# Kernel optimization log

Hardware: AMD Instinct MI355X
Metric: run time of the kernel (lower is better)

The kernel has to match this reference:

```python
import jax, jax.numpy as jnp
import numpy as np
import math

MUL = 32
E = 131072
N = 10000
IRREPS = [(0, 1), (1, -1), (2, 1)]  # (l, parity) for 0e + 1o + 2e
SQRT3 = math.sqrt(3.0)

_f = math.factorial


def _w3j_symbol(j1, j2, j3, m1, m2, m3):
    """Standard (complex-basis) Wigner 3j symbol via the Racah formula."""
    if m1 + m2 + m3 != 0:
        return 0.0
    if abs(m1) > j1 or abs(m2) > j2 or abs(m3) > j3:
        return 0.0
    if not (abs(j1 - j2) <= j3 <= j1 + j2):
        return 0.0
    tri = _f(j1 + j2 - j3) * _f(j1 - j2 + j3) * _f(-j1 + j2 + j3) / _f(j1 + j2 + j3 + 1)
    pref = (-1) ** (j1 - j2 - m3) * math.sqrt(
        tri * _f(j1 + m1) * _f(j1 - m1) * _f(j2 + m2) * _f(j2 - m2) * _f(j3 + m3) * _f(j3 - m3)
    )
    tmin = max(0, j2 - j3 - m1, j1 - j3 + m2)
    tmax = min(j1 + j2 - j3, j1 - m1, j2 + m2)
    s = 0.0
    for t in range(tmin, tmax + 1):
        s += (-1) ** t / (
            _f(t) * _f(j3 - j2 + t + m1) * _f(j3 - j1 + t - m2)
            * _f(j1 + j2 - j3 - t) * _f(j1 - t - m1) * _f(j2 - t + m2)
        )
    return pref * s


def _real_basis(l):
    """Complex -> real spherical-harmonic change of basis, rows m=-l..l."""
    U = np.zeros((2 * l + 1, 2 * l + 1), dtype=np.complex128)
    U[l, l] = 1.0
    s = 1.0 / math.sqrt(2.0)
    for m in range(1, l + 1):
        U[l + m, l + m] = ((-1) ** m) * s
        U[l + m, l - m] = s
        U[l - m, l - m] = 1j * s
        U[l - m, l + m] = -1j * ((-1) ** m) * s
    return U


def _w3j_real(l1, l2, l3):
    """Real-basis Wigner 3j tensor, Frobenius norm 1 (e3nn normalization)."""
    Wc = np.zeros((2 * l1 + 1, 2 * l2 + 1, 2 * l3 + 1), dtype=np.complex128)
    for m1 in range(-l1, l1 + 1):
        for m2 in range(-l2, l2 + 1):
            for m3 in range(-l3, l3 + 1):
                Wc[l1 + m1, l2 + m2, l3 + m3] = _w3j_symbol(l1, l2, l3, m1, m2, m3)
    C = np.einsum('im,jn,ko,mno->ijk', _real_basis(l1), _real_basis(l2), _real_basis(l3), Wc)
    re, im = C.real, C.imag
    R = re if np.linalg.norm(re) >= np.linalg.norm(im) else im
    return R / np.linalg.norm(R)


def _build_w3j():
    dims = [2 * l + 1 for l, _ in IRREPS]
    offs = np.concatenate([[0], np.cumsum(dims)])[:-1]
    base_dim = int(sum(dims))  # 9
    # auto-generated instructions: same loop order as the torch module
    ins = []
    for io, (lo, po) in enumerate(IRREPS):
        for i1, (l1, p1) in enumerate(IRREPS):
            for i2, (l2, p2) in enumerate(IRREPS):
                if p1 * p2 == po and abs(l1 - l2) <= lo <= l1 + l2:
                    ins.append((i1, i2, io))
    P = len(ins)  # 11 paths
    w3j = np.zeros((P, base_dim, base_dim, base_dim), dtype=np.float32)
    for p, (i1, i2, io) in enumerate(ins):
        l1, l2, lo = IRREPS[i1][0], IRREPS[i2][0], IRREPS[io][0]
        C = _w3j_real(l1, l2, lo) * math.sqrt(2 * lo + 1)  # component normalization
        w3j[p, offs[i1]:offs[i1] + dims[i1], offs[i2]:offs[i2] + dims[i2], offs[io]:offs[io] + dims[io]] = C
    return w3j


def setup_inputs() -> dict:
    key = jax.random.key(0)
    k1, k2, k3, k4 = jax.random.split(key, 4)
    w3j = jnp.asarray(_build_w3j())  # [P=11, 9, 9, 9]
    P = w3j.shape[0]
    base_dim = w3j.shape[1]
    return {
        'x1': jax.random.normal(k1, (E, MUL * base_dim), dtype=jnp.float32),
        'x2': jax.random.normal(k2, (E, MUL * base_dim), dtype=jnp.float32),
        'idxs': jax.random.randint(k3, (E,), 0, N),
        'weights': jax.random.uniform(k4, (MUL, P), dtype=jnp.float32, minval=-SQRT3, maxval=SQRT3),
        'w3j': w3j,
        'scatter_dim_size': N,
    }


def reference(x1, x2, idxs, weights, w3j, scatter_dim_size):
    base1 = w3j.shape[1]
    base2 = w3j.shape[2]
    # scatter edges -> nodes, then gather back per edge (neighbor sum per center)
    x2s = jax.ops.segment_sum(x2, idxs, num_segments=int(scatter_dim_size))
    x2g = x2s[idxs]
    x1r = x1.reshape(-1, MUL, base1)   # [E, u, i]
    x2r = x2g.reshape(-1, MUL, base2)  # [E, u, j]
    # path-channel coupled weighting: 'up,pijk->uijk'
    ww3j = jnp.einsum('up,pijk->uijk', weights, w3j)
    # out[e,u,k] = sum_ij x1[e,u,i] x2[e,u,j] ww3j[u,i,j,k]
    out = jnp.einsum('eui,euj,uijk->euk', x1r, x2r, ww3j)
    return out
```

## Files before the change

kernel.cpp:

```cpp
#include <hip/hip_runtime.h>

#define MULV 32
#define BASE 9
#define ROW 288
#define NPATH 11
#define W3J_SZ 729
#define PACK_STRIDE 96
#define PACK_TOTAL (MULV * PACK_STRIDE)
#define TILE 64
#define QCOL 72
#define LSTR 73
#define NQ4 18
#define QTOT (TILE * NQ4)

typedef float f4a4 __attribute__((ext_vector_type(4), aligned(4)));

__device__ constexpr int p_o1[NPATH] = {0,1,4, 0,1,1,4, 0,1,4,4};
__device__ constexpr int p_d1[NPATH] = {1,3,5, 1,3,3,5, 1,3,5,5};
__device__ constexpr int p_o2[NPATH] = {0,1,4, 1,0,4,1, 4,1,0,4};
__device__ constexpr int p_d2[NPATH] = {1,3,5, 3,1,5,3, 5,3,1,5};
__device__ constexpr int p_o3[NPATH] = {0,0,0, 1,1,1,1, 4,4,4,4};
__device__ constexpr int p_d3[NPATH] = {1,1,1, 3,3,3,3, 5,5,5,5};
__device__ constexpr int p_l1[NPATH] = {0,1,2, 0,1,1,2, 0,1,2,2};
__device__ constexpr int p_l2[NPATH] = {0,1,2, 1,0,2,1, 2,1,0,2};
__device__ constexpr int p_l3[NPATH] = {0,0,0, 1,1,1,1, 2,2,2,2};

__device__ __host__ constexpr bool cell_nz(int p, int i, int j, int k) {
    int m1 = i - p_l1[p], m2 = j - p_l2[p], m3 = k - p_l3[p];
    if ((((m1 < 0) + (m2 < 0) + (m3 < 0)) & 1) != 0) return false;
    int a1 = m1 < 0 ? -m1 : m1, a2 = m2 < 0 ? -m2 : m2, a3 = m3 < 0 ? -m3 : m3;
    int d = a1 - a2; if (d < 0) d = -d;
    return (a3 == a1 + a2) || (a3 == d);
}
__device__ __host__ constexpr bool pair_nz(int p, int i, int j) {
    for (int k = 0; k < p_d3[p]; ++k) if (cell_nz(p, i, j, k)) return true;
    return false;
}


__global__ void zero_count_kernel(float* __restrict__ ws, const int* __restrict__ dN) {
    int N = dN[0];
    int* count = (int*)(ws + PACK_TOTAL + (long)N * ROW);
    for (int i = blockIdx.x * blockDim.x + threadIdx.x; i < N; i += gridDim.x * blockDim.x)
        count[i] = 0;
}

__global__ void hist_kernel(const int* __restrict__ idxs, float* __restrict__ ws,
                            const int* __restrict__ dN, int E) {
    int N = dN[0];
    int* count = (int*)(ws + PACK_TOTAL + (long)N * ROW);
    int t = blockIdx.x * blockDim.x + threadIdx.x;
    if (t < E) atomicAdd(&count[idxs[t]], 1);
}

__global__ void scan_kernel(float* __restrict__ ws, const int* __restrict__ dN) {
    int N = dN[0];
    int* count  = (int*)(ws + PACK_TOTAL + (long)N * ROW);
    int* offset = count + N;
    int* cursor = count + 2 * N;
    __shared__ int tsum[1024];
    const int tid = threadIdx.x;
    int cpt = (N + 1023) / 1024;
    int lo = tid * cpt;
    int hi = lo + cpt; if (hi > N) hi = N;
    int s = 0;
    for (int i = lo; i < hi; ++i) s += count[i];
    int v = s;
    tsum[tid] = v;
    __syncthreads();
    #pragma unroll
    for (int off = 1; off < 1024; off <<= 1) {
        int t = (tid >= off) ? tsum[tid - off] : 0;
        __syncthreads();
        v += t;
        tsum[tid] = v;
        __syncthreads();
    }
    int run = v - s;
    for (int i = lo; i < hi; ++i) {
        int c = count[i];
        offset[i] = run; cursor[i] = run;
        run += c;
    }
}

__global__ void fill_kernel(const int* __restrict__ idxs, float* __restrict__ ws,
                            const int* __restrict__ dN, int E) {
    int N = dN[0];
    int* count  = (int*)(ws + PACK_TOTAL + (long)N * ROW);
    int* cursor = count + 2 * N;
    int* bucket = count + 3 * N;
    int t = blockIdx.x * blockDim.x + threadIdx.x;
    if (t < E) {
        int n = idxs[t];
        int pos = atomicAdd(&cursor[n], 1);
        bucket[pos] = t;
    }
}

__global__ __launch_bounds__(256) void gather_sum_kernel(const float* __restrict__ x2,
                                                         float* __restrict__ ws,
                                                         const int* __restrict__ dN) {
    int N = dN[0];
    float* x2s  = ws + PACK_TOTAL;
    int* count  = (int*)(x2s + (long)N * ROW);
    int* offset = count + N;
    int* bucket = count + 3 * N;
    const int lane = threadIdx.x & 63;
    const int wv   = threadIdx.x >> 6;
    for (int n0 = blockIdx.x * 4 + wv; n0 < N; n0 += gridDim.x * 4) {
        int n   = __builtin_amdgcn_readfirstlane(n0);
        int off = offset[n];
        int deg = count[n];
        float4 a0 = make_float4(0.f, 0.f, 0.f, 0.f);
        float4 a1 = make_float4(0.f, 0.f, 0.f, 0.f);
        int d = 0;
        for (; d + 4 <= deg; d += 4) {
            int e0 = bucket[off + d + 0];
            int e1 = bucket[off + d + 1];
            int e2 = bucket[off + d + 2];
            int e3 = bucket[off + d + 3];
            const float4* r0 = (const float4*)(x2 + (long)e0 * ROW);
            const float4* r1 = (const float4*)(x2 + (long)e1 * ROW);
            const float4* r2 = (const float4*)(x2 + (long)e2 * ROW);
            const float4* r3 = (const float4*)(x2 + (long)e3 * ROW);
            float4 v0 = r0[lane], v1 = r1[lane], v2 = r2[lane], v3 = r3[lane];
            float4 w0, w1, w2, w3;
            if (lane < 8) {
                w0 = r0[64 + lane]; w1 = r1[64 + lane];
                w2 = r2[64 + lane]; w3 = r3[64 + lane];
            }
            a0.x += v0.x + v1.x + v2.x + v3.x;
            a0.y += v0.y + v1.y + v2.y + v3.y;
            a0.z += v0.z + v1.z + v2.z + v3.z;
            a0.w += v0.w + v1.w + v2.w + v3.w;
            if (lane < 8) {
                a1.x += w0.x + w1.x + w2.x + w3.x;
                a1.y += w0.y + w1.y + w2.y + w3.y;
                a1.z += w0.z + w1.z + w2.z + w3.z;
                a1.w += w0.w + w1.w + w2.w + w3.w;
            }
        }
        for (; d < deg; ++d) {
            int e = bucket[off + d];
            const float4* row = (const float4*)(x2 + (long)e * ROW);
            float4 v = row[lane];
            a0.x += v.x; a0.y += v.y; a0.z += v.z; a0.w += v.w;
            if (lane < 8) {
                float4 w = row[64 + lane];
                a1.x += w.x; a1.y += w.y; a1.z += w.z; a1.w += w.w;
            }
        }
        float4* orow = (float4*)(x2s + (long)n * ROW);
        orow[lane] = a0;
        if (lane < 8) orow[64 + lane] = a1;
    }
}

__global__ void ww_build_kernel(const float* __restrict__ weights,
                                const float* __restrict__ w3j,
                                float* __restrict__ packed) {
    int u = threadIdx.x;
    if (u >= MULV) return;
    int ci = 0;
    #pragma unroll
    for (int p = 0; p < NPATH; ++p) {
        float wgt = weights[u * NPATH + p];
        #pragma unroll
        for (int i = 0; i < p_d1[p]; ++i)
            #pragma unroll
            for (int j = 0; j < p_d2[p]; ++j)
                #pragma unroll
                for (int k = 0; k < p_d3[p]; ++k)
                    if (cell_nz(p, i, j, k)) {
                        int idx = (p_o1[p] + i) * 81 + (p_o2[p] + j) * 9 + (p_o3[p] + k);
                        packed[u * PACK_STRIDE + ci] = wgt * w3j[p * W3J_SZ + idx];
                        ++ci;
                    }
    }
}

template <bool GUARD>
__global__ __launch_bounds__(256, 4) void contract_kernel(
    const float* __restrict__ x1, const int* __restrict__ idxs,
    float* __restrict__ ws, const int* __restrict__ dN,
    float* __restrict__ out, int E)
{
    __shared__ float tile[TILE * LSTR];
    const int tid = threadIdx.x;
    const int ebase = blockIdx.x * TILE;
    const float* __restrict__ packed = ws;
    const float* __restrict__ x2s    = ws + PACK_TOTAL;

    int rr[5], cc4[5];
    bool ok[5];
    #pragma unroll
    for (int t = 0; t < 5; ++t) {
        int q = tid + t * 256;
        int r = q / NQ4;
        rr[t] = r; cc4[t] = q - r * NQ4;
        ok[t] = (q < QTOT) && (!GUARD || (ebase + r) < E);
    }

    const int lane = tid & 63;
    const int wv   = __builtin_amdgcn_readfirstlane(tid >> 6);
    int ecomp = ebase + lane;
    if (GUARD && ecomp >= E) ecomp = E - 1;
    const int n = idxs[ecomp];
    const float* __restrict__ r2 = x2s + (long)n * ROW;
    float* __restrict__ lrow = &tile[lane * LSTR];

    float4 buf[5];
    #pragma unroll
    for (int t = 0; t < 5; ++t)
        if (ok[t])
            buf[t] = *(const float4*)(x1 + (long)(ebase + rr[t]) * ROW + cc4[t] * 4);

    float x2c[BASE];
    {
        const float* s = r2 + wv * BASE;
        f4a4 a = *(const f4a4*)s;
        f4a4 b = *(const f4a4*)(s + 4);
        x2c[0]=a.x; x2c[1]=a.y; x2c[2]=a.z; x2c[3]=a.w;
        x2c[4]=b.x; x2c[5]=b.y; x2c[6]=b.z; x2c[7]=b.w;
        x2c[8]=s[8];
    }

    #pragma unroll 1
    for (int h = 0; h < 4; ++h) {
        #pragma unroll
        for (int t = 0; t < 5; ++t) {
            if (ok[t]) {
                float* d = &tile[rr[t] * LSTR + cc4[t] * 4];
                d[0] = buf[t].x; d[1] = buf[t].y; d[2] = buf[t].z; d[3] = buf[t].w;
            }
        }
        __syncthreads();

        if (h < 3) {
            #pragma unroll
            for (int t = 0; t < 5; ++t)
                if (ok[t])
                    buf[t] = *(const float4*)(x1 + (long)(ebase + rr[t]) * ROW
                                              + (h + 1) * QCOL + cc4[t] * 4);
        }

        #pragma unroll 1
        for (int c = 0; c < 2; ++c) {
            const int u = 8 * h + c * 4 + wv;
            const float* __restrict__ wp = packed + u * PACK_STRIDE;

            float x2n[BASE];
            if (u + 4 < MULV) {
                const float* s = r2 + (u + 4) * BASE;
                f4a4 a = *(const f4a4*)s;
                f4a4 b = *(const f4a4*)(s + 4);
                x2n[0]=a.x; x2n[1]=a.y; x2n[2]=a.z; x2n[3]=a.w;
                x2n[4]=b.x; x2n[5]=b.y; x2n[6]=b.z; x2n[7]=b.w;
                x2n[8]=s[8];
            }

            const int lbase = (c * 4 + wv) * BASE;
            float x1v[BASE], acc[BASE];
            #pragma unroll
            for (int i = 0; i < BASE; ++i) {
                x1v[i] = lrow[lbase + i];
                acc[i] = 0.0f;
            }

            int ci = 0;
            #pragma unroll
            for (int p = 0; p < NPATH; ++p) {
                #pragma unroll
                for (int i = 0; i < p_d1[p]; ++i) {
                    #pragma unroll
                    for (int j = 0; j < p_d2[p]; ++j) {
                        if (pair_nz(p, i, j)) {
                            float xx = x1v[p_o1[p] + i] * x2c[p_o2[p] + j];
                            #pragma unroll
                            for (int k = 0; k < p_d3[p]; ++k) {
                                if (cell_nz(p, i, j, k)) {
                                    acc[p_o3[p] + k] = fmaf(wp[ci], xx, acc[p_o3[p] + k]);
                                    ++ci;
                                }
                            }
                        }
                    }
                }
            }
            #pragma unroll
            for (int k = 0; k < BASE; ++k)
                lrow[lbase + k] = acc[k];
            if (u + 4 < MULV) {
                #pragma unroll
                for (int i = 0; i < BASE; ++i) x2c[i] = x2n[i];
            }
        }
        __syncthreads();

        #pragma unroll
        for (int t = 0; t < 5; ++t) {
            if (ok[t]) {
                const float* s = &tile[rr[t] * LSTR + cc4[t] * 4];
                *(float4*)(out + (long)(ebase + rr[t]) * ROW + h * QCOL + cc4[t] * 4) =
                    make_float4(s[0], s[1], s[2], s[3]);
            }
        }
    }
}

extern "C" void kernel_launch(void* const* d_in, const int* in_sizes, int n_in,
                              void* d_out, int out_size, void* d_ws, size_t ws_size,
                              hipStream_t stream) {
    const float* x1      = (const float*)d_in[0];
    const float* x2      = (const float*)d_in[1];
    const int*   idxs    = (const int*)d_in[2];
    const float* weights = (const float*)d_in[3];
    const float* w3j     = (const float*)d_in[4];
    const int*   dN      = (const int*)d_in[5];
    float* out = (float*)d_out;
    float* ws  = (float*)d_ws;

    const int E = in_sizes[2];
    const int eb = (E + 255) / 256;

    zero_count_kernel<<<256, 256, 0, stream>>>(ws, dN);
    hist_kernel<<<eb, 256, 0, stream>>>(idxs, ws, dN, E);
    scan_kernel<<<1, 1024, 0, stream>>>(ws, dN);
    fill_kernel<<<eb, 256, 0, stream>>>(idxs, ws, dN, E);

    gather_sum_kernel<<<2500, 256, 0, stream>>>(x2, ws, dN);

    ww_build_kernel<<<1, 64, 0, stream>>>(weights, w3j, ws);

    if (E % TILE == 0) {
        contract_kernel<false><<<E / TILE, 256, 0, stream>>>(x1, idxs, ws, dN, out, E);
    } else {
        contract_kernel<true><<<(E + TILE - 1) / TILE, 256, 0, stream>>>(x1, idxs, ws, dN, out, E);
    }
}
```

Measured before the change: 183.9 us.

## Stage gathered x2 rows through LDS with coalesced loads instead of per-lane reads

The gathered x2 node rows are now loaded cooperatively as coalesced float4 chunks into a second shared-memory tile, matching the staging already used for x1. Before, each lane read its own 9-float slice straight from global memory and prefetched the next one. Node indices are first placed in shared memory so every thread can compute the gather addresses. This drops the register prefetch of x1 across h iterations, so loads are no longer overlapped with compute. It also doubles LDS use per block, which may reduce occupancy.

```diff
diff --git a/kernel.cpp b/kernel.cpp
--- a/kernel.cpp
+++ b/kernel.cpp
@@ -186,11 +186,20 @@
     float* __restrict__ ws, const int* __restrict__ dN,
     float* __restrict__ out, int E)
 {
-    __shared__ float tile[TILE * LSTR];
+    __shared__ float lx1[TILE * LSTR];
+    __shared__ float lx2[TILE * LSTR];
+    __shared__ int ln[TILE];
     const int tid = threadIdx.x;
     const int ebase = blockIdx.x * TILE;
     const float* __restrict__ packed = ws;
     const float* __restrict__ x2s    = ws + PACK_TOTAL;
+
+    if (tid < TILE) {
+        int ee = ebase + tid;
+        if (GUARD && ee >= E) ee = E - 1;
+        ln[tid] = idxs[ee];
+    }
+    __syncthreads();
 
     int rr[5], cc4[5];
     bool ok[5];
@@ -201,70 +210,48 @@
         rr[t] = r; cc4[t] = q - r * NQ4;
         ok[t] = (q < QTOT) && (!GUARD || (ebase + r) < E);
     }
+    int nn[5];
+    #pragma unroll
+    for (int t = 0; t < 5; ++t) nn[t] = ok[t] ? ln[rr[t]] : 0;
 
     const int lane = tid & 63;
     const int wv   = __builtin_amdgcn_readfirstlane(tid >> 6);
-    int ecomp = ebase + lane;
-    if (GUARD && ecomp >= E) ecomp = E - 1;
-    const int n = idxs[ecomp];
-    const float* __restrict__ r2 = x2s + (long)n * ROW;
-    float* __restrict__ lrow = &tile[lane * LSTR];
-
-    float4 buf[5];
-    #pragma unroll
-    for (int t = 0; t < 5; ++t)
-        if (ok[t])
-            buf[t] = *(const float4*)(x1 + (long)(ebase + rr[t]) * ROW + cc4[t] * 4);
-
-    float x2c[BASE];
-    {
-        const float* s = r2 + wv * BASE;
-        f4a4 a = *(const f4a4*)s;
-        f4a4 b = *(const f4a4*)(s + 4);
-        x2c[0]=a.x; x2c[1]=a.y; x2c[2]=a.z; x2c[3]=a.w;
-        x2c[4]=b.x; x2c[5]=b.y; x2c[6]=b.z; x2c[7]=b.w;
-        x2c[8]=s[8];
-    }
+    const float* __restrict__ l1row = &lx1[lane * LSTR];
+    const float* __restrict__ l2row = &lx2[lane * LSTR];
 
     #pragma unroll 1
     for (int h = 0; h < 4; ++h) {
         #pragma unroll
         for (int t = 0; t < 5; ++t) {
             if (ok[t]) {
-                float* d = &tile[rr[t] * LSTR + cc4[t] * 4];
-                d[0] = buf[t].x; d[1] = buf[t].y; d[2] = buf[t].z; d[3] = buf[t].w;
+                float4 v = *(const float4*)(x1 + (long)(ebase + rr[t]) * ROW
+                                            + h * QCOL + cc4[t] * 4);
+                float* d = &lx1[rr[t] * LSTR + cc4[t] * 4];
+                d[0] = v.x; d[1] = v.y; d[2] = v.z; d[3] = v.w;
+            }
+        }
+        #pragma unroll
+        for (int t = 0; t < 5; ++t) {
+            if (ok[t]) {
+                float4 v = *(const float4*)(x2s + (long)nn[t] * ROW
+                                            + h * QCOL + cc4[t] * 4);
+                float* d = &lx2[rr[t] * LSTR + cc4[t] * 4];
+                d[0] = v.x; d[1] = v.y; d[2] = v.z; d[3] = v.w;
             }
         }
         __syncthreads();
-
-        if (h < 3) {
-            #pragma unroll
-            for (int t = 0; t < 5; ++t)
-                if (ok[t])
-                    buf[t] = *(const float4*)(x1 + (long)(ebase + rr[t]) * ROW
-                                              + (h + 1) * QCOL + cc4[t] * 4);
-        }
 
         #pragma unroll 1
         for (int c = 0; c < 2; ++c) {
             const int u = 8 * h + c * 4 + wv;
             const float* __restrict__ wp = packed + u * PACK_STRIDE;
-
-            float x2n[BASE];
-            if (u + 4 < MULV) {
-                const float* s = r2 + (u + 4) * BASE;
-                f4a4 a = *(const f4a4*)s;
-                f4a4 b = *(const f4a4*)(s + 4);
-                x2n[0]=a.x; x2n[1]=a.y; x2n[2]=a.z; x2n[3]=a.w;
-                x2n[4]=b.x; x2n[5]=b.y; x2n[6]=b.z; x2n[7]=b.w;
-                x2n[8]=s[8];
-            }
-
             const int lbase = (c * 4 + wv) * BASE;
-            float x1v[BASE], acc[BASE];
+
+            float x1v[BASE], x2v[BASE], acc[BASE];
             #pragma unroll
             for (int i = 0; i < BASE; ++i) {
-                x1v[i] = lrow[lbase + i];
+                x1v[i] = l1row[lbase + i];
+                x2v[i] = l2row[lbase + i];
                 acc[i] = 0.0f;
             }
 
@@ -276,7 +263,7 @@
                     #pragma unroll
                     for (int j = 0; j < p_d2[p]; ++j) {
                         if (pair_nz(p, i, j)) {
-                            float xx = x1v[p_o1[p] + i] * x2c[p_o2[p] + j];
+                            float xx = x1v[p_o1[p] + i] * x2v[p_o2[p] + j];
                             #pragma unroll
                             for (int k = 0; k < p_d3[p]; ++k) {
                                 if (cell_nz(p, i, j, k)) {
@@ -288,20 +275,16 @@
                     }
                 }
             }
+            float* wdst = &lx1[lane * LSTR + lbase];
             #pragma unroll
-            for (int k = 0; k < BASE; ++k)
-                lrow[lbase + k] = acc[k];
-            if (u + 4 < MULV) {
-                #pragma unroll
-                for (int i = 0; i < BASE; ++i) x2c[i] = x2n[i];
-            }
+            for (int k = 0; k < BASE; ++k) wdst[k] = acc[k];
         }
         __syncthreads();
 
         #pragma unroll
         for (int t = 0; t < 5; ++t) {
             if (ok[t]) {
-                const float* s = &tile[rr[t] * LSTR + cc4[t] * 4];
+                const float* s = &lx1[rr[t] * LSTR + cc4[t] * 4];
                 *(float4*)(out + (long)(ebase + rr[t]) * ROW + h * QCOL + cc4[t] * 4) =
                     make_float4(s[0], s[1], s[2], s[3]);
             }
```

Result: slower. 189.2 us (+2.9%).
